# Kernel optimization log

Hardware: AMD Instinct MI355X
Metric: run time of the kernel (lower is better)

## Reference

```python
import jax, jax.numpy as jnp
import numpy as np

NUM_LEVELS = 3
K = 512
COMMIT = (0.25, 0.5, 1.0)
DECAY = 0.99
EPS = 1e-05


def setup_inputs() -> dict:
    key = jax.random.key(0)
    k1, k2, k3 = jax.random.split(key, 3)
    z_e = jax.random.normal(k1, (16, 4096, 1024), dtype=jnp.float32)
    codebooks = jax.random.normal(k2, (NUM_LEVELS, K, 1024), dtype=jnp.float32)
    ema_cluster = jnp.ones((NUM_LEVELS, K), dtype=jnp.float32)
    ema_w = jax.random.normal(k3, (NUM_LEVELS, K, 1024), dtype=jnp.float32)
    return {"z_e": z_e, "codebooks": codebooks, "ema_cluster": ema_cluster, "ema_w": ema_w}


def reference(z_e, codebooks, ema_cluster, ema_w):
    """Hierarchical residual VQ: 3 levels of cdist+argmin+gather, residual subtract,
    commitment loss, and EMA codebook update stats via scatter-add (segment_sum)."""
    B, T, D = z_e.shape
    flat = z_e.reshape(-1, D)  # [N, D]
    residual = flat
    z_q = jnp.zeros_like(flat)
    loss = jnp.zeros((), dtype=flat.dtype)
    idx_list = []
    new_codebooks = []

    for l in range(NUM_LEVELS):
        C = codebooks[l]  # [K, D]
        # squared euclidean distances [N, K] (expanded form, no NxKxD intermediate)
        d = (jnp.sum(residual * residual, axis=-1, keepdims=True)
             - 2.0 * residual @ C.T
             + jnp.sum(C * C, axis=-1))
        idx = jnp.argmin(d, axis=-1)  # [N] nearest code
        q = C[idx]  # gather [N, D]

        # commitment loss (EMA-style VQ: no gradient codebook loss)
        loss = loss + COMMIT[l] * jnp.mean((residual - jax.lax.stop_gradient(q)) ** 2)

        # EMA codebook update statistics (scatter-add, no grad)
        r_sg = jax.lax.stop_gradient(residual)
        counts = jax.ops.segment_sum(jnp.ones((r_sg.shape[0],), dtype=flat.dtype), idx, num_segments=K)
        sums = jax.ops.segment_sum(r_sg, idx, num_segments=K)  # [K, D]
        cs = DECAY * ema_cluster[l] + (1.0 - DECAY) * counts
        w = DECAY * ema_w[l] + (1.0 - DECAY) * sums
        n = jnp.sum(cs)
        cs_norm = (cs + EPS) / (n + K * EPS) * n  # laplace smoothing
        new_codebooks.append(w / cs_norm[:, None])

        residual = residual - q
        z_q = z_q + q
        idx_list.append(idx)

    # straight-through estimator
    z_q_st = flat + jax.lax.stop_gradient(z_q - flat)
    indices = jnp.stack(idx_list).reshape(NUM_LEVELS, B, T)
    return z_q_st.reshape(B, T, D), loss, indices, jnp.stack(new_codebooks)
```

## Files before the change

kernel.cpp:

```cpp
#include <hip/hip_runtime.h>

#define NPTS   65536
#define DIM    1024
#define NCODE  512
#define NLVL   3

#define ZQ_OFF   0
#define LOSS_OFF 67108864
#define IDX_OFF  67108865
#define CB_OFF   67305473

#define PB    128
#define CBCH  256
#define KS    32
#define NTHR2 512

typedef unsigned short u16;
typedef unsigned int   u32;
typedef __attribute__((ext_vector_type(8))) short short8;
typedef __attribute__((ext_vector_type(4))) float f32x4;

__device__ inline void merge_top2(float& v1, int& i1, float& v2, int& i2,
                                  float w1, int j1, float w2, int j2) {
    bool aFirst = (v1 < w1) || (v1 == w1 && i1 < j1);
    float t1v = aFirst ? v1 : w1; int t1i = aFirst ? i1 : j1;
    float c1v = aFirst ? v2 : w2; int c1i = aFirst ? i2 : j2;
    float c2v = aFirst ? w1 : v1; int c2i = aFirst ? j1 : i1;
    bool cFirst = (c1v < c2v) || (c1v == c2v && c1i < c2i);
    v1 = t1v; i1 = t1i;
    v2 = cFirst ? c1v : c2v;
    i2 = cFirst ? c1i : c2i;
}

__device__ inline u16 bf16_rne(float x) {
    u32 u = __float_as_uint(x);
    u32 r = u + 0x7fffu + ((u >> 16) & 1u);
    return (u16)(r >> 16);
}
__device__ inline float bf16_f(u16 h) { return __uint_as_float(((u32)h) << 16); }

__device__ inline void gload_lds16(const void* g, void* l) {
    __builtin_amdgcn_global_load_lds((const __attribute__((address_space(1))) void*)g,
                                     (__attribute__((address_space(3))) void*)l, 16, 0, 0);
}

__global__ __launch_bounds__(256) void cnorm_kernel(const float* __restrict__ cb,
                                                    float* __restrict__ cnorm) {
    __shared__ float sd[256];
    const int b = blockIdx.x;
    const int tid = threadIdx.x;
    const float4 v = *(const float4*)&cb[(size_t)b * DIM + tid * 4];
    sd[tid] = v.x*v.x + v.y*v.y + v.z*v.z + v.w*v.w;
    __syncthreads();
    for (int o = 128; o > 0; o >>= 1) { if (tid < o) sd[tid] += sd[tid+o]; __syncthreads(); }
    if (tid == 0) cnorm[b] = sd[0];
}

__global__ __launch_bounds__(256) void cvtcb_kernel(const float* __restrict__ cbs,
                                                    char* __restrict__ planes) {
    const int b = blockIdx.x;
    const int tid = threadIdx.x;
    const int l = b >> 9, k = b & 511;
    u16* ph = (u16*)(planes + (size_t)l * 2097152);
    u16* pl = ph + NCODE * DIM;
    const float4 v = *(const float4*)&cbs[(size_t)b * DIM + tid * 4];
    float xs[4] = {v.x, v.y, v.z, v.w};
    u16 hh[4], ll[4];
    #pragma unroll
    for (int e = 0; e < 4; ++e) {
        hh[e] = bf16_rne(xs[e]);
        ll[e] = bf16_rne(xs[e] - bf16_f(hh[e]));
    }
    *(ushort4*)&ph[(size_t)k * DIM + tid * 4] = make_ushort4(hh[0], hh[1], hh[2], hh[3]);
    *(ushort4*)&pl[(size_t)k * DIM + tid * 4] = make_ushort4(ll[0], ll[1], ll[2], ll[3]);
}

__global__ __launch_bounds__(512, 4) void level_kernel(
        const float* __restrict__ r_in,
        float* __restrict__ r_out,
        const float* __restrict__ cbf,
        const u16* __restrict__ cb_h,
        const u16* __restrict__ cb_l,
        const float* __restrict__ cnorm_l,
        float* __restrict__ out_idx_f,
        int*   __restrict__ ws_idx,
        float* __restrict__ loss_partial)
{
    __shared__ union {
        struct {
            u16 A[2][CBCH][KS];
            u16 B[2][PB][KS];
        } st;
        struct {
            float4 top[4][PB];
            double ref[PB][2][2];
            int    i1[PB], i2[PB], w[PB];
            float  red[NTHR2];
        } tl;
    } sm;
    __shared__ float s_cn[NCODE];

    const int tid  = threadIdx.x;
    const int lane = tid & 63;
    const int wid  = tid >> 6;
    const int wm   = wid >> 1;
    const int wn   = wid & 1;
    const int g    = lane >> 4;
    const int l15  = lane & 15;
    const int fr   = (l15 >> 1) & 3;
    const int pbase = blockIdx.x * PB;

    u16* sAf = &sm.st.A[0][0][0];
    u16* sBf = &sm.st.B[0][0][0];

    s_cn[tid] = cnorm_l[tid];

    float bv1[4], bv2[4]; int bi1[4], bi2[4];
    #pragma unroll
    for (int i = 0; i < 4; ++i) { bv1[i] = 1e30f; bv2[i] = 1e30f; bi1[i] = 0; bi2[i] = 1; }

    const u16* srcp = (wid < 4) ? cb_h : cb_l;

    for (int ch = 0; ch < 2; ++ch) {
        const int cbase = ch * CBCH;
        f32x4 acc[4][4] = {};

        for (int ks0 = 0; ks0 < DIM; ks0 += KS) {
            __syncthreads();

            #pragma unroll
            for (int j = 0; j < 4; ++j) {
                const int c   = wid * 256 + j * 64 + lane;
                const int cc  = c & 1023;
                const int row = cc >> 2, slot = cc & 3;
                const u16* gp = srcp + (size_t)(cbase + row) * DIM + ks0
                                + ((slot ^ ((row >> 1) & 3)) << 3);
                gload_lds16(gp, sAf + (size_t)c * 8);
            }

            {
                const int row = tid >> 2, slot = tid & 3;
                const float* gp = r_in + (size_t)(pbase + row) * DIM + ks0 + slot * 8;
                const float4 a0 = *(const float4*)gp;
                const float4 a1 = *(const float4*)(gp + 4);
                float xs[8] = {a0.x, a0.y, a0.z, a0.w, a1.x, a1.y, a1.z, a1.w};
                short8 h8, l8;
                #pragma unroll
                for (int e = 0; e < 8; ++e) {
                    const u16 hb = bf16_rne(xs[e]);
                    const u16 lb = bf16_rne(xs[e] - bf16_f(hb));
                    h8[e] = (short)hb; l8[e] = (short)lb;
                }
                const int woff = row * KS + ((slot ^ ((row >> 1) & 3)) << 3);
                *(short8*)(sBf + woff) = h8;
                *(short8*)(sBf + 4096 + woff) = l8;
            }
            asm volatile("s_waitcnt vmcnt(0)" ::: "memory");
            __syncthreads();

            {
                const int ksl = (g ^ fr) << 3;
                short8 bh[4], bl[4];
                #pragma unroll
                for (int nf = 0; nf < 4; ++nf) {
                    const int row = wn * 64 + nf * 16 + l15;
                    bh[nf] = *(const short8*)(sBf + row * KS + ksl);
                    bl[nf] = *(const short8*)(sBf + 4096 + row * KS + ksl);
                }
                #pragma unroll
                for (int mf = 0; mf < 4; ++mf) {
                    const int row = wm * 64 + mf * 16 + l15;
                    const short8 ah = *(const short8*)(sAf + row * KS + ksl);
                    const short8 al = *(const short8*)(sAf + 8192 + row * KS + ksl);
                    #pragma unroll
                    for (int nf = 0; nf < 4; ++nf) {
                        acc[mf][nf] = __builtin_amdgcn_mfma_f32_16x16x32_bf16(ah, bh[nf], acc[mf][nf], 0, 0, 0);
                        acc[mf][nf] = __builtin_amdgcn_mfma_f32_16x16x32_bf16(ah, bl[nf], acc[mf][nf], 0, 0, 0);
                        acc[mf][nf] = __builtin_amdgcn_mfma_f32_16x16x32_bf16(al, bh[nf], acc[mf][nf], 0, 0, 0);
                    }
                }
            }
        }

        #pragma unroll
        for (int nf = 0; nf < 4; ++nf)
            #pragma unroll
            for (int mf = 0; mf < 4; ++mf)
                #pragma unroll
                for (int r = 0; r < 4; ++r) {
                    const int code = cbase + wm * 64 + mf * 16 + g * 4 + r;
                    const float sv = s_cn[code] - 2.0f * acc[mf][nf][r];
                    if (sv < bv1[nf])      { bv2[nf] = bv1[nf]; bi2[nf] = bi1[nf]; bv1[nf] = sv; bi1[nf] = code; }
                    else if (sv < bv2[nf]) { bv2[nf] = sv; bi2[nf] = code; }
                }
    }

    __syncthreads();

    #pragma unroll
    for (int nf = 0; nf < 4; ++nf) {
        float v1 = bv1[nf], v2 = bv2[nf]; int i1 = bi1[nf], i2 = bi2[nf];
        #pragma unroll
        for (int m = 16; m < 64; m <<= 1) {
            const float w1 = __shfl_xor(v1, m); const int j1 = __shfl_xor(i1, m);
            const float w2 = __shfl_xor(v2, m); const int j2 = __shfl_xor(i2, m);
            merge_top2(v1, i1, v2, i2, w1, j1, w2, j2);
        }
        if (g == 0)
            sm.tl.top[wm][wn * 64 + nf * 16 + l15] =
                make_float4(v1, __int_as_float(i1), v2, __int_as_float(i2));
    }
    __syncthreads();

    if (tid < PB) {
        float4 t = sm.tl.top[0][tid];
        float v1 = t.x; int i1 = __float_as_int(t.y);
        float v2 = t.z; int i2 = __float_as_int(t.w);
        #pragma unroll
        for (int wmm = 1; wmm < 4; ++wmm) {
            const float4 u = sm.tl.top[wmm][tid];
            merge_top2(v1, i1, v2, i2, u.x, __float_as_int(u.y), u.z, __float_as_int(u.w));
        }
        sm.tl.i1[tid] = i1; sm.tl.i2[tid] = i2;
    }
    __syncthreads();

    {
        const int p = tid >> 2, cand = (tid >> 1) & 1, half = tid & 1;
        const int k = cand ? sm.tl.i2[p] : sm.tl.i1[p];
        const float4* rr = (const float4*)(r_in + (size_t)(pbase + p) * DIM + half * 512);
        const float4* cr = (const float4*)(cbf + (size_t)k * DIM + half * 512);
        double s0 = 0.0, s1 = 0.0, s2 = 0.0, s3 = 0.0;
        for (int d = 0; d < 128; ++d) {
            const float4 c4 = cr[d];
            const float4 r4 = rr[d];
            s0 += (double)c4.x * ((double)c4.x - 2.0 * (double)r4.x);
            s1 += (double)c4.y * ((double)c4.y - 2.0 * (double)r4.y);
            s2 += (double)c4.z * ((double)c4.z - 2.0 * (double)r4.z);
            s3 += (double)c4.w * ((double)c4.w - 2.0 * (double)r4.w);
        }
        sm.tl.ref[p][cand][half] = (s0 + s1) + (s2 + s3);
    }
    __syncthreads();
    if (tid < PB) {
        const double sA_ = sm.tl.ref[tid][0][0] + sm.tl.ref[tid][0][1];
        const double sB_ = sm.tl.ref[tid][1][0] + sm.tl.ref[tid][1][1];
        const int iA = sm.tl.i1[tid], iB = sm.tl.i2[tid];
        const int w = (sB_ < sA_ || (sB_ == sA_ && iB < iA)) ? iB : iA;
        sm.tl.w[tid] = w;
        out_idx_f[pbase + tid] = (float)w;
        ws_idx[pbase + tid] = w;
    }
    __syncthreads();

    float lsum = 0.f;
    const int colb = (tid & 255) * 4;
    const int phh  = tid >> 8;
    for (int pp = 0; pp < PB; pp += 2) {
        const int p = pp + phh;
        const int w = sm.tl.w[p];
        const size_t off = (size_t)(pbase + p) * DIM + colb;
        const float4 rv = *(const float4*)&r_in[off];
        const float4 cv = *(const float4*)&cbf[(size_t)w * DIM + colb];
        float4 rn;
        rn.x = rv.x - cv.x; rn.y = rv.y - cv.y; rn.z = rv.z - cv.z; rn.w = rv.w - cv.w;
        if (r_out) *(float4*)&r_out[off] = rn;
        lsum += rn.x*rn.x + rn.y*rn.y + rn.z*rn.z + rn.w*rn.w;
    }
    sm.tl.red[tid] = lsum;
    __syncthreads();
    for (int o = 256; o > 0; o >>= 1) { if (tid < o) sm.tl.red[tid] += sm.tl.red[tid + o]; __syncthreads(); }
    if (tid == 0) loss_partial[blockIdx.x] = sm.tl.red[0];
}

#define SCHUNK 4096
__global__ __launch_bounds__(256) void sums_kernel(
        const int* __restrict__ idx, const float* __restrict__ src,
        const float* __restrict__ cb, int addC,
        float* __restrict__ sums_out, int* __restrict__ counts_out)
{
    __shared__ int s_idx[SCHUNK];
    __shared__ int s_list[SCHUNK];
    __shared__ int s_scan[256];
    const int k = blockIdx.x, tid = threadIdx.x;
    float4 acc = make_float4(0.f, 0.f, 0.f, 0.f);
    int nk = 0;
    for (int base = 0; base < NPTS; base += SCHUNK) {
        __syncthreads();
        for (int j = tid; j < SCHUNK; j += 256) s_idx[j] = idx[base + j];
        __syncthreads();
        int cnt = 0;
        const int S = SCHUNK / 256;
        #pragma unroll
        for (int j = 0; j < S; ++j) cnt += (s_idx[tid * S + j] == k);
        s_scan[tid] = cnt;
        __syncthreads();
        for (int off = 1; off < 256; off <<= 1) {
            int v = (tid >= off) ? s_scan[tid - off] : 0;
            __syncthreads();
            s_scan[tid] += v;
            __syncthreads();
        }
        const int total = s_scan[255];
        int pos = s_scan[tid] - cnt;
        for (int j = 0; j < S; ++j)
            if (s_idx[tid * S + j] == k) s_list[pos++] = base + tid * S + j;
        __syncthreads();
        for (int j = 0; j < total; ++j) {
            const int pid = s_list[j];
            float4 v = *(const float4*)&src[(size_t)pid * DIM + tid * 4];
            acc.x += v.x; acc.y += v.y; acc.z += v.z; acc.w += v.w;
        }
        nk += total;
    }
    if (addC) {
        float4 c = *(const float4*)&cb[(size_t)k * DIM + tid * 4];
        float fn = (float)nk;
        acc.x += fn * c.x; acc.y += fn * c.y; acc.z += fn * c.z; acc.w += fn * c.w;
    }
    *(float4*)&sums_out[(size_t)k * DIM + tid * 4] = acc;
    if (tid == 0) counts_out[k] = nk;
}

__global__ __launch_bounds__(256) void zq_kernel(const float* __restrict__ z_e,
                                                 const float* __restrict__ cb2,
                                                 const int* __restrict__ idx2,
                                                 float* __restrict__ zq) {
    const int total = NPTS * (DIM / 4);
    for (int i = blockIdx.x * 256 + threadIdx.x; i < total; i += gridDim.x * 256) {
        const size_t e = (size_t)i * 4;
        const int p = (int)(e >> 10);
        const int d = (int)(e & 1023);
        const int w = idx2[p];
        float4 z = *(const float4*)&z_e[e];
        float4 r = *(const float4*)&zq[e];
        float4 c = *(const float4*)&cb2[(size_t)w * DIM + d];
        float4 o;
        o.x = z.x - r.x + c.x; o.y = z.y - r.y + c.y;
        o.z = z.z - r.z + c.z; o.w = z.w - r.w + c.w;
        *(float4*)&zq[e] = o;
    }
}

__global__ __launch_bounds__(512) void nsum_kernel(const float* __restrict__ ec,
                                                   const int* __restrict__ counts,
                                                   float* __restrict__ n_ws) {
    __shared__ float sd[512];
    const int l = blockIdx.x, tid = threadIdx.x;
    sd[tid] = 0.99f * ec[l * NCODE + tid] + 0.01f * (float)counts[l * NCODE + tid];
    __syncthreads();
    for (int o = 256; o > 0; o >>= 1) { if (tid < o) sd[tid] += sd[tid+o]; __syncthreads(); }
    if (tid == 0) n_ws[l] = sd[0];
}

__global__ __launch_bounds__(256) void newcb_kernel(const float* __restrict__ ema_w,
                                                    const float* __restrict__ sums,
                                                    const float* __restrict__ ec,
                                                    const int* __restrict__ counts,
                                                    const float* __restrict__ n_ws,
                                                    float* __restrict__ out_cb) {
    const int b = blockIdx.x;
    const int tid = threadIdx.x;
    const int l = b >> 9;
    const float cs = 0.99f * ec[b] + 0.01f * (float)counts[b];
    const float n = n_ws[l];
    const float csn = (cs + 1e-5f) / (n + 512.0f * 1e-5f) * n;
    const size_t off = (size_t)b * DIM + tid * 4;
    float4 w = *(const float4*)&ema_w[off];
    float4 s4 = *(const float4*)&sums[off];
    float4 o;
    o.x = (0.99f * w.x + 0.01f * s4.x) / csn;
    o.y = (0.99f * w.y + 0.01f * s4.y) / csn;
    o.z = (0.99f * w.z + 0.01f * s4.z) / csn;
    o.w = (0.99f * w.w + 0.01f * s4.w) / csn;
    *(float4*)&out_cb[off] = o;
}

__global__ __launch_bounds__(256) void loss_kernel(const float* __restrict__ lp,
                                                   float* __restrict__ out_loss) {
    __shared__ double sd[256];
    const int tid = threadIdx.x;
    const double commit[3] = {0.25, 0.5, 1.0};
    double acc = 0.0;
    for (int l = 0; l < NLVL; ++l) {
        double s = 0.0;
        for (int j = tid; j < 512; j += 256) s += (double)lp[l * 512 + j];
        sd[tid] = s;
        __syncthreads();
        for (int o = 128; o > 0; o >>= 1) { if (tid < o) sd[tid] += sd[tid+o]; __syncthreads(); }
        if (tid == 0) acc += commit[l] * sd[0] / 67108864.0;
        __syncthreads();
    }
    if (tid == 0) *out_loss = (float)acc;
}

extern "C" void kernel_launch(void* const* d_in, const int* in_sizes, int n_in,
                              void* d_out, int out_size, void* d_ws, size_t ws_size,
                              hipStream_t stream) {
    const float* z_e   = (const float*)d_in[0];
    const float* cbs   = (const float*)d_in[1];
    const float* ema_c = (const float*)d_in[2];
    const float* ema_w = (const float*)d_in[3];
    float* out = (float*)d_out;

    char* ws = (char*)d_ws;
    int*   ws_idx = (int*)ws;
    float* cnorm  = (float*)(ws + 786432);
    int*   counts = (int*)(ws + 792576);
    float* lossp  = (float*)(ws + 798720);
    float* n_ws   = (float*)(ws + 811008);
    float* sums   = (float*)(ws + 811024);
    char*  planes = (char*)(ws + 811024);

    float* zq       = out + ZQ_OFF;
    float* out_loss = out + LOSS_OFF;
    float* out_idx  = out + IDX_OFF;
    float* out_cb   = out + CB_OFF;

    const float* cb0 = cbs;
    const float* cb1 = cbs + (size_t)1 * NCODE * DIM;
    const float* cb2 = cbs + (size_t)2 * NCODE * DIM;

    u16* ph0 = (u16*)(planes);                     u16* pl0 = ph0 + NCODE * DIM;
    u16* ph1 = (u16*)(planes + 2097152);           u16* pl1 = ph1 + NCODE * DIM;
    u16* ph2 = (u16*)(planes + 2 * 2097152);       u16* pl2 = ph2 + NCODE * DIM;

    cvtcb_kernel<<<NLVL * NCODE, 256, 0, stream>>>(cbs, planes);
    cnorm_kernel<<<NLVL * NCODE, 256, 0, stream>>>(cbs, cnorm);

    level_kernel<<<NPTS / PB, NTHR2, 0, stream>>>(z_e, zq, cb0, ph0, pl0, cnorm,
                                                  out_idx, ws_idx, lossp);
    sums_kernel<<<NCODE, 256, 0, stream>>>(ws_idx, z_e, nullptr, 0,
                                           sums, counts);
    level_kernel<<<NPTS / PB, NTHR2, 0, stream>>>(zq, zq, cb1, ph1, pl1, cnorm + NCODE,
                                                  out_idx + NPTS, ws_idx + NPTS, lossp + 512);
    sums_kernel<<<NCODE, 256, 0, stream>>>(ws_idx + NPTS, zq, cb1, 1,
                                           sums + (size_t)NCODE * DIM, counts + NCODE);
    level_kernel<<<NPTS / PB, NTHR2, 0, stream>>>(zq, nullptr, cb2, ph2, pl2, cnorm + 2 * NCODE,
                                                  out_idx + 2 * NPTS, ws_idx + 2 * NPTS, lossp + 1024);
    sums_kernel<<<NCODE, 256, 0, stream>>>(ws_idx + 2 * NPTS, zq, nullptr, 0,
                                           sums + (size_t)2 * NCODE * DIM, counts + 2 * NCODE);
    zq_kernel<<<4096, 256, 0, stream>>>(z_e, cb2, ws_idx + 2 * NPTS, zq);

    nsum_kernel<<<NLVL, 512, 0, stream>>>(ema_c, counts, n_ws);
    newcb_kernel<<<NLVL * NCODE, 256, 0, stream>>>(ema_w, sums, ema_c, counts, n_ws, out_cb);
    loss_kernel<<<1, 256, 0, stream>>>(lossp, out_loss);
}
```

Before: 2.648 ms.

## Double-buffer level GEMM pipeline, unroll sums gather, fuse zq into final sums

The level kernel's distance GEMM now runs as one flattened loop over code chunks of 128 with double-buffered LDS tiles. The next codebook tile and the residual tile two steps ahead are prefetched while the current one is multiplied, using a single barrier per step and raised wave priority around the MFMAs. The sums kernel unrolls its gather-accumulate by four with independent accumulators for more memory parallelism. The final level's sums pass also writes z_q in place, replacing the separate full-size zq kernel pass. Smaller accumulator tiles cut register pressure but double the top-2 selection work, and the hand-placed waitcnt counts must be exactly right.

```diff
diff --git a/kernel.cpp b/kernel.cpp
--- a/kernel.cpp
+++ b/kernel.cpp
@@ -11,8 +11,9 @@
 #define CB_OFF   67305473
 
 #define PB    128
-#define CBCH  256
+#define CBCH  128
 #define KS    32
+#define NITER 128
 #define NTHR2 512
 
 typedef unsigned short u16;
@@ -88,8 +89,8 @@
 {
     __shared__ union {
         struct {
-            u16 A[2][CBCH][KS];
-            u16 B[2][PB][KS];
+            u16 A[2][2][CBCH][KS];
+            u16 B[2][2][PB][KS];
         } st;
         struct {
             float4 top[4][PB];
@@ -108,91 +109,134 @@
     const int g    = lane >> 4;
     const int l15  = lane & 15;
     const int fr   = (l15 >> 1) & 3;
+    const int ksl  = (g ^ fr) << 3;
     const int pbase = blockIdx.x * PB;
 
-    u16* sAf = &sm.st.A[0][0][0];
-    u16* sBf = &sm.st.B[0][0][0];
+    u16* sAf = &sm.st.A[0][0][0][0];
 
     s_cn[tid] = cnorm_l[tid];
+
+    const u16* srcp = (wid < 4) ? cb_h : cb_l;
+    const int c0 = wid * 128 + lane;
+    const int c1 = c0 + 64;
+    const int ar0 = (c0 & 511) >> 2, as0 = (((c0 & 3) ^ ((ar0 >> 1) & 3)) << 3);
+    const int ar1 = (c1 & 511) >> 2, as1 = (((c1 & 3) ^ ((ar1 >> 1) & 3)) << 3);
+    const u16* aptr0 = srcp + (size_t)ar0 * DIM + as0;
+    const u16* aptr1 = srcp + (size_t)ar1 * DIM + as1;
+    const int aldst0 = c0 * 8, aldst1 = c1 * 8;
+
+    const int brow = tid >> 2, bslot = tid & 3;
+    const float* bsrc = r_in + (size_t)(pbase + brow) * DIM + bslot * 8;
+    const int bwoff = brow * KS + (((bslot ^ ((brow >> 1) & 3))) << 3);
 
     float bv1[4], bv2[4]; int bi1[4], bi2[4];
     #pragma unroll
     for (int i = 0; i < 4; ++i) { bv1[i] = 1e30f; bv2[i] = 1e30f; bi1[i] = 0; bi2[i] = 1; }
 
-    const u16* srcp = (wid < 4) ? cb_h : cb_l;
-
-    for (int ch = 0; ch < 2; ++ch) {
-        const int cbase = ch * CBCH;
-        f32x4 acc[4][4] = {};
-
-        for (int ks0 = 0; ks0 < DIM; ks0 += KS) {
-            __syncthreads();
-
+    f32x4 acc[2][4];
+    #pragma unroll
+    for (int mf = 0; mf < 2; ++mf)
+        #pragma unroll
+        for (int nf = 0; nf < 4; ++nf) acc[mf][nf] = (f32x4)0.0f;
+
+    float4 pX0, pX1, pY0, pY1;
+
+    gload_lds16(aptr0, sAf + aldst0);
+    gload_lds16(aptr1, sAf + aldst1);
+    __builtin_amdgcn_sched_barrier(0);
+    {
+        const float4 b00 = *(const float4*)(bsrc);
+        const float4 b01 = *(const float4*)(bsrc + 4);
+        pX0 = *(const float4*)(bsrc + 32);
+        pX1 = *(const float4*)(bsrc + 36);
+        float xs[8] = {b00.x, b00.y, b00.z, b00.w, b01.x, b01.y, b01.z, b01.w};
+        short8 h8, l8;
+        #pragma unroll
+        for (int e = 0; e < 8; ++e) {
+            const u16 hb = bf16_rne(xs[e]);
+            const u16 lb = bf16_rne(xs[e] - bf16_f(hb));
+            h8[e] = (short)hb; l8[e] = (short)lb;
+        }
+        u16* sBw = sAf + 16384;
+        *(short8*)(sBw + bwoff) = h8;
+        *(short8*)(sBw + 4096 + bwoff) = l8;
+    }
+    asm volatile("s_waitcnt vmcnt(0) lgkmcnt(0)" ::: "memory");
+    __builtin_amdgcn_s_barrier();
+    __builtin_amdgcn_sched_barrier(0);
+
+    auto body = [&](const int it, const int CUR,
+                    float4& ld0, float4& ld1, float4& cv0, float4& cv1) {
+        const int nxt  = (it + 1) & (NITER - 1);
+        const int goff = (nxt >> 5) * (CBCH * DIM) + ((nxt & 31) << 5);
+        gload_lds16(aptr0 + goff, sAf + (CUR ^ 1) * 8192 + aldst0);
+        gload_lds16(aptr1 + goff, sAf + (CUR ^ 1) * 8192 + aldst1);
+        __builtin_amdgcn_sched_barrier(0);
+        const int koff2 = ((it + 2) & 31) << 5;
+        ld0 = *(const float4*)(bsrc + koff2);
+        ld1 = *(const float4*)(bsrc + koff2 + 4);
+        const u16* bA = sAf + CUR * 8192;
+        const u16* bB = sAf + 16384 + CUR * 8192;
+        short8 ah[2], al[2];
+        #pragma unroll
+        for (int mf = 0; mf < 2; ++mf) {
+            const int row = wm * 32 + mf * 16 + l15;
+            ah[mf] = *(const short8*)(bA + row * KS + ksl);
+            al[mf] = *(const short8*)(bA + 4096 + row * KS + ksl);
+        }
+        __builtin_amdgcn_s_setprio(1);
+        #pragma unroll
+        for (int nf = 0; nf < 4; ++nf) {
+            const int row = wn * 64 + nf * 16 + l15;
+            const short8 bh = *(const short8*)(bB + row * KS + ksl);
+            const short8 bl = *(const short8*)(bB + 4096 + row * KS + ksl);
             #pragma unroll
-            for (int j = 0; j < 4; ++j) {
-                const int c   = wid * 256 + j * 64 + lane;
-                const int cc  = c & 1023;
-                const int row = cc >> 2, slot = cc & 3;
-                const u16* gp = srcp + (size_t)(cbase + row) * DIM + ks0
-                                + ((slot ^ ((row >> 1) & 3)) << 3);
-                gload_lds16(gp, sAf + (size_t)c * 8);
+            for (int mf = 0; mf < 2; ++mf) {
+                acc[mf][nf] = __builtin_amdgcn_mfma_f32_16x16x32_bf16(ah[mf], bh, acc[mf][nf], 0, 0, 0);
+                acc[mf][nf] = __builtin_amdgcn_mfma_f32_16x16x32_bf16(ah[mf], bl, acc[mf][nf], 0, 0, 0);
+                acc[mf][nf] = __builtin_amdgcn_mfma_f32_16x16x32_bf16(al[mf], bh, acc[mf][nf], 0, 0, 0);
             }
-
-            {
-                const int row = tid >> 2, slot = tid & 3;
-                const float* gp = r_in + (size_t)(pbase + row) * DIM + ks0 + slot * 8;
-                const float4 a0 = *(const float4*)gp;
-                const float4 a1 = *(const float4*)(gp + 4);
-                float xs[8] = {a0.x, a0.y, a0.z, a0.w, a1.x, a1.y, a1.z, a1.w};
-                short8 h8, l8;
+        }
+        __builtin_amdgcn_s_setprio(0);
+        {
+            float xs[8] = {cv0.x, cv0.y, cv0.z, cv0.w, cv1.x, cv1.y, cv1.z, cv1.w};
+            short8 h8, l8;
+            #pragma unroll
+            for (int e = 0; e < 8; ++e) {
+                const u16 hb = bf16_rne(xs[e]);
+                const u16 lb = bf16_rne(xs[e] - bf16_f(hb));
+                h8[e] = (short)hb; l8[e] = (short)lb;
+            }
+            u16* sBw = sAf + 16384 + (CUR ^ 1) * 8192;
+            *(short8*)(sBw + bwoff) = h8;
+            *(short8*)(sBw + 4096 + bwoff) = l8;
+        }
+        if ((it & 31) == 31) {
+            const int cbase = (it >> 5) * CBCH;
+            #pragma unroll
+            for (int nf = 0; nf < 4; ++nf)
                 #pragma unroll
-                for (int e = 0; e < 8; ++e) {
-                    const u16 hb = bf16_rne(xs[e]);
-                    const u16 lb = bf16_rne(xs[e] - bf16_f(hb));
-                    h8[e] = (short)hb; l8[e] = (short)lb;
-                }
-                const int woff = row * KS + ((slot ^ ((row >> 1) & 3)) << 3);
-                *(short8*)(sBf + woff) = h8;
-                *(short8*)(sBf + 4096 + woff) = l8;
-            }
-            asm volatile("s_waitcnt vmcnt(0)" ::: "memory");
-            __syncthreads();
-
-            {
-                const int ksl = (g ^ fr) << 3;
-                short8 bh[4], bl[4];
+                for (int mf = 0; mf < 2; ++mf)
+                    #pragma unroll
+                    for (int r = 0; r < 4; ++r) {
+                        const int code = cbase + wm * 32 + mf * 16 + g * 4 + r;
+                        const float sv = s_cn[code] - 2.0f * acc[mf][nf][r];
+                        if (sv < bv1[nf])      { bv2[nf] = bv1[nf]; bi2[nf] = bi1[nf]; bv1[nf] = sv; bi1[nf] = code; }
+                        else if (sv < bv2[nf]) { bv2[nf] = sv; bi2[nf] = code; }
+                    }
+            #pragma unroll
+            for (int mf = 0; mf < 2; ++mf)
                 #pragma unroll
-                for (int nf = 0; nf < 4; ++nf) {
-                    const int row = wn * 64 + nf * 16 + l15;
-                    bh[nf] = *(const short8*)(sBf + row * KS + ksl);
-                    bl[nf] = *(const short8*)(sBf + 4096 + row * KS + ksl);
-                }
-                #pragma unroll
-                for (int mf = 0; mf < 4; ++mf) {
-                    const int row = wm * 64 + mf * 16 + l15;
-                    const short8 ah = *(const short8*)(sAf + row * KS + ksl);
-                    const short8 al = *(const short8*)(sAf + 8192 + row * KS + ksl);
-                    #pragma unroll
-                    for (int nf = 0; nf < 4; ++nf) {
-                        acc[mf][nf] = __builtin_amdgcn_mfma_f32_16x16x32_bf16(ah, bh[nf], acc[mf][nf], 0, 0, 0);
-                        acc[mf][nf] = __builtin_amdgcn_mfma_f32_16x16x32_bf16(ah, bl[nf], acc[mf][nf], 0, 0, 0);
-                        acc[mf][nf] = __builtin_amdgcn_mfma_f32_16x16x32_bf16(al, bh[nf], acc[mf][nf], 0, 0, 0);
-                    }
-                }
-            }
-        }
-
-        #pragma unroll
-        for (int nf = 0; nf < 4; ++nf)
-            #pragma unroll
-            for (int mf = 0; mf < 4; ++mf)
-                #pragma unroll
-                for (int r = 0; r < 4; ++r) {
-                    const int code = cbase + wm * 64 + mf * 16 + g * 4 + r;
-                    const float sv = s_cn[code] - 2.0f * acc[mf][nf][r];
-                    if (sv < bv1[nf])      { bv2[nf] = bv1[nf]; bi2[nf] = bi1[nf]; bv1[nf] = sv; bi1[nf] = code; }
-                    else if (sv < bv2[nf]) { bv2[nf] = sv; bi2[nf] = code; }
-                }
+                for (int nf = 0; nf < 4; ++nf) acc[mf][nf] = (f32x4)0.0f;
+        }
+        asm volatile("s_waitcnt vmcnt(2) lgkmcnt(0)" ::: "memory");
+        __builtin_amdgcn_s_barrier();
+        __builtin_amdgcn_sched_barrier(0);
+    };
+
+    for (int it2 = 0; it2 < NITER; it2 += 2) {
+        body(it2,     0, pY0, pY1, pX0, pX1);
+        body(it2 + 1, 1, pX0, pX1, pY0, pY1);
     }
 
     __syncthreads();
@@ -277,13 +321,16 @@
 __global__ __launch_bounds__(256) void sums_kernel(
         const int* __restrict__ idx, const float* __restrict__ src,
         const float* __restrict__ cb, int addC,
-        float* __restrict__ sums_out, int* __restrict__ counts_out)
+        float* __restrict__ sums_out, int* __restrict__ counts_out,
+        const float* __restrict__ ze, float* __restrict__ zqout)
 {
     __shared__ int s_idx[SCHUNK];
     __shared__ int s_list[SCHUNK];
     __shared__ int s_scan[256];
     const int k = blockIdx.x, tid = threadIdx.x;
-    float4 acc = make_float4(0.f, 0.f, 0.f, 0.f);
+    float4 a0 = make_float4(0.f,0.f,0.f,0.f), a1 = a0, a2 = a0, a3 = a0;
+    float4 cbrow = make_float4(0.f,0.f,0.f,0.f);
+    if (cb) cbrow = *(const float4*)&cb[(size_t)k * DIM + tid * 4];
     int nk = 0;
     for (int base = 0; base < NPTS; base += SCHUNK) {
         __syncthreads();
@@ -306,40 +353,66 @@
         for (int j = 0; j < S; ++j)
             if (s_idx[tid * S + j] == k) s_list[pos++] = base + tid * S + j;
         __syncthreads();
-        for (int j = 0; j < total; ++j) {
-            const int pid = s_list[j];
-            float4 v = *(const float4*)&src[(size_t)pid * DIM + tid * 4];
-            acc.x += v.x; acc.y += v.y; acc.z += v.z; acc.w += v.w;
+        int j = 0;
+        for (; j + 4 <= total; j += 4) {
+            const size_t o0 = (size_t)s_list[j]   * DIM + tid * 4;
+            const size_t o1 = (size_t)s_list[j+1] * DIM + tid * 4;
+            const size_t o2 = (size_t)s_list[j+2] * DIM + tid * 4;
+            const size_t o3 = (size_t)s_list[j+3] * DIM + tid * 4;
+            const float4 v0 = *(const float4*)&src[o0];
+            const float4 v1 = *(const float4*)&src[o1];
+            const float4 v2 = *(const float4*)&src[o2];
+            const float4 v3 = *(const float4*)&src[o3];
+            a0.x += v0.x; a0.y += v0.y; a0.z += v0.z; a0.w += v0.w;
+            a1.x += v1.x; a1.y += v1.y; a1.z += v1.z; a1.w += v1.w;
+            a2.x += v2.x; a2.y += v2.y; a2.z += v2.z; a2.w += v2.w;
+            a3.x += v3.x; a3.y += v3.y; a3.z += v3.z; a3.w += v3.w;
+            if (zqout) {
+                const float4 z0 = *(const float4*)&ze[o0];
+                const float4 z1 = *(const float4*)&ze[o1];
+                const float4 z2 = *(const float4*)&ze[o2];
+                const float4 z3 = *(const float4*)&ze[o3];
+                float4 q;
+                q.x = z0.x - v0.x + cbrow.x; q.y = z0.y - v0.y + cbrow.y;
+                q.z = z0.z - v0.z + cbrow.z; q.w = z0.w - v0.w + cbrow.w;
+                *(float4*)&zqout[o0] = q;
+                q.x = z1.x - v1.x + cbrow.x; q.y = z1.y - v1.y + cbrow.y;
+                q.z = z1.z - v1.z + cbrow.z; q.w = z1.w - v1.w + cbrow.w;
+                *(float4*)&zqout[o1] = q;
+                q.x = z2.x - v2.x + cbrow.x; q.y = z2.y - v2.y + cbrow.y;
+                q.z = z2.z - v2.z + cbrow.z; q.w = z2.w - v2.w + cbrow.w;
+                *(float4*)&zqout[o2] = q;
+                q.x = z3.x - v3.x + cbrow.x; q.y = z3.y - v3.y + cbrow.y;
+                q.z = z3.z - v3.z + cbrow.z; q.w = z3.w - v3.w + cbrow.w;
+                *(float4*)&zqout[o3] = q;
+            }
+        }
+        for (; j < total; ++j) {
+            const size_t o0 = (size_t)s_list[j] * DIM + tid * 4;
+            const float4 v0 = *(const float4*)&src[o0];
+            a0.x += v0.x; a0.y += v0.y; a0.z += v0.z; a0.w += v0.w;
+            if (zqout) {
+                const float4 z0 = *(const float4*)&ze[o0];
+                float4 q;
+                q.x = z0.x - v0.x + cbrow.x; q.y = z0.y - v0.y + cbrow.y;
+                q.z = z0.z - v0.z + cbrow.z; q.w = z0.w - v0.w + cbrow.w;
+                *(float4*)&zqout[o0] = q;
+            }
         }
         nk += total;
     }
+    float4 acc;
+    acc.x = (a0.x + a1.x) + (a2.x + a3.x);
+    acc.y = (a0.y + a1.y) + (a2.y + a3.y);
+    acc.z = (a0.z + a1.z) + (a2.z + a3.z);
+    acc.w = (a0.w + a1.w) + (a2.w + a3.w);
     if (addC) {
-        float4 c = *(const float4*)&cb[(size_t)k * DIM + tid * 4];
-        float fn = (float)nk;
-        acc.x += fn * c.x; acc.y += fn * c.y; acc.z += fn * c.z; acc.w += fn * c.w;
+        const float fn = (float)nk;
+        acc.x += fn * cbrow.x; acc.y += fn * cbrow.y;
+        acc.z += fn * cbrow.z; acc.w += fn * cbrow.w;
     }
     *(float4*)&sums_out[(size_t)k * DIM + tid * 4] = acc;
     if (tid == 0) counts_out[k] = nk;
-}
-
-__global__ __launch_bounds__(256) void zq_kernel(const float* __restrict__ z_e,
-                                                 const float* __restrict__ cb2,
-                                                 const int* __restrict__ idx2,
-                                                 float* __restrict__ zq) {
-    const int total = NPTS * (DIM / 4);
-    for (int i = blockIdx.x * 256 + threadIdx.x; i < total; i += gridDim.x * 256) {
-        const size_t e = (size_t)i * 4;
-        const int p = (int)(e >> 10);
-        const int d = (int)(e & 1023);
-        const int w = idx2[p];
-        float4 z = *(const float4*)&z_e[e];
-        float4 r = *(const float4*)&zq[e];
-        float4 c = *(const float4*)&cb2[(size_t)w * DIM + d];
-        float4 o;
-        o.x = z.x - r.x + c.x; o.y = z.y - r.y + c.y;
-        o.z = z.z - r.z + c.z; o.w = z.w - r.w + c.w;
-        *(float4*)&zq[e] = o;
-    }
 }
 
 __global__ __launch_bounds__(512) void nsum_kernel(const float* __restrict__ ec,
@@ -431,16 +504,17 @@
     level_kernel<<<NPTS / PB, NTHR2, 0, stream>>>(z_e, zq, cb0, ph0, pl0, cnorm,
                                                   out_idx, ws_idx, lossp);
     sums_kernel<<<NCODE, 256, 0, stream>>>(ws_idx, z_e, nullptr, 0,
-                                           sums, counts);
+                                           sums, counts, nullptr, nullptr);
     level_kernel<<<NPTS / PB, NTHR2, 0, stream>>>(zq, zq, cb1, ph1, pl1, cnorm + NCODE,
                                                   out_idx + NPTS, ws_idx + NPTS, lossp + 512);
     sums_kernel<<<NCODE, 256, 0, stream>>>(ws_idx + NPTS, zq, cb1, 1,
-                                           sums + (size_t)NCODE * DIM, counts + NCODE);
+                                           sums + (size_t)NCODE * DIM, counts + NCODE,
+                                           nullptr, nullptr);
     level_kernel<<<NPTS / PB, NTHR2, 0, stream>>>(zq, nullptr, cb2, ph2, pl2, cnorm + 2 * NCODE,
                                                   out_idx + 2 * NPTS, ws_idx + 2 * NPTS, lossp + 1024);
-    sums_kernel<<<NCODE, 256, 0, stream>>>(ws_idx + 2 * NPTS, zq, nullptr, 0,
-                                           sums + (size_t)2 * NCODE * DIM, counts + 2 * NCODE);
-    zq_kernel<<<4096, 256, 0, stream>>>(z_e, cb2, ws_idx + 2 * NPTS, zq);
+    sums_kernel<<<NCODE, 256, 0, stream>>>(ws_idx + 2 * NPTS, zq, cb2, 0,
+                                           sums + (size_t)2 * NCODE * DIM, counts + 2 * NCODE,
+                                           z_e, zq);
 
     nsum_kernel<<<NLVL, 512, 0, stream>>>(ema_c, counts, n_ws);
     newcb_kernel<<<NLVL * NCODE, 256, 0, stream>>>(ema_w, sums, ema_c, counts, n_ws, out_cb);
```

After: 3.448 ms. 30.2% more time.
